# Optimization experiments

Hardware: AMD Instinct MI355X
Metric: run time of the kernel (lower is better)

## Reference

```python
import jax, jax.numpy as jnp
import numpy as np

B, T, E, H = 4, 2048, 1024, 16
HS = E // H  # head_size = 64


def setup_inputs() -> dict:
    key = jax.random.key(0)
    ks = jax.random.split(key, 5)
    x = jax.random.normal(ks[0], (B, T, E), jnp.float32)
    scale = 0.02
    Wq = jax.random.normal(ks[1], (H, E, HS), jnp.float32) * scale
    Wk = jax.random.normal(ks[2], (H, E, HS), jnp.float32) * scale
    Wv = jax.random.normal(ks[3], (H, E, HS), jnp.float32) * scale
    Wo = jax.random.normal(ks[4], (E, E), jnp.float32) * scale
    bo = jnp.zeros((E,), jnp.float32)
    return {"x": x, "Wq": Wq, "Wk": Wk, "Wv": Wv, "Wo": Wo, "bo": bo}


def reference(x, Wq, Wk, Wv, Wo, bo):
    b, t, e = x.shape
    # per-head projections, batched over heads
    Q = jnp.einsum('bte,hed->bhtd', x, Wq)  # (B,H,T,HS)
    K = jnp.einsum('bte,hed->bhtd', x, Wk)
    V = jnp.einsum('bte,hed->bhtd', x, Wv)
    # faithful quirk 1: scale by sqrt(embd_size), not sqrt(head_size)
    scores = jnp.einsum('bhtd,bhsd->bhts', Q, K) / jnp.sqrt(jnp.float32(e))
    mask = jnp.tril(jnp.ones((t, t), dtype=bool))  # (T_q, T_k)
    scores = jnp.where(mask[None, None, :, :], scores, -jnp.inf)
    # faithful quirk 2: original softmaxes over dim=1 of (B,Tq,Tk) = the QUERY axis
    attn = jax.nn.softmax(scores, axis=2)
    out = jnp.einsum('bhts,bhsd->bhtd', attn, V)  # (B,H,T,HS)
    out = out.transpose(0, 2, 1, 3).reshape(b, t, e)  # concat heads -> (B,T,E)
    return out @ Wo + bo
```

## Files before the change

### kernel.cpp

```cpp
#include <hip/hip_runtime.h>
#include <stdint.h>

#define Bn 4
#define Tn 2048
#define En 1024
#define Hn 16
#define HSn 64
#define BHn (Bn*Hn)
#define NRn (Bn*Tn)

#define CEXP 0.0450840831f

typedef __attribute__((ext_vector_type(8))) short short8;
typedef __attribute__((ext_vector_type(4))) float f32x4;
typedef __attribute__((ext_vector_type(16))) float f32x16;
typedef __attribute__((ext_vector_type(4))) unsigned int uint4w;

__device__ __forceinline__ unsigned short f2b(float f){
  union { float f; unsigned int u; } c; c.f = f;
  unsigned int u = c.u + 0x7FFFu + ((c.u >> 16) & 1u);
  return (unsigned short)(u >> 16);
}
__device__ __forceinline__ float b2f(unsigned short s){
  union { unsigned int u; float f; } c; c.u = ((unsigned int)s) << 16;
  return c.f;
}
__device__ __forceinline__ unsigned int cvtpk(float lo, float hi){
  unsigned int r;
  asm("v_cvt_pk_bf16_f32 %0, %1, %2" : "=v"(r) : "v"(lo), "v"(hi));
  return r;
}
__device__ __forceinline__ f32x4 mfma16(short8 a, short8 b, f32x4 c){
  return __builtin_amdgcn_mfma_f32_16x16x32_bf16(a, b, c, 0, 0, 0);
}
__device__ __forceinline__ f32x16 mfma32(short8 a, short8 b, f32x16 c){
  return __builtin_amdgcn_mfma_f32_32x32x16_bf16(a, b, c, 0, 0, 0);
}
__device__ __forceinline__ void gl16(const void* g, void* s){
  __builtin_amdgcn_global_load_lds((const __attribute__((address_space(1))) unsigned int*)g,
                                   (__attribute__((address_space(3))) unsigned int*)s, 16, 0, 0);
}
#define FENCE()    asm volatile("" ::: "memory")
#define WAITV(N)   asm volatile("s_waitcnt vmcnt(" #N ")" ::: "memory")
#define SBAR()     __builtin_amdgcn_s_barrier()

__global__ void k_cvt_x(const float* __restrict__ x, unsigned short* __restrict__ xb){
  int i = (blockIdx.x * blockDim.x + threadIdx.x) * 8;
  float4 a = *(const float4*)(x + i);
  float4 b = *(const float4*)(x + i + 4);
  alignas(16) unsigned short o[8] = {f2b(a.x),f2b(a.y),f2b(a.z),f2b(a.w),
                                     f2b(b.x),f2b(b.y),f2b(b.z),f2b(b.w)};
  *(uint4w*)(xb + i) = *(const uint4w*)o;
}

__global__ void k_wT(const float* __restrict__ Wq, const float* __restrict__ Wk,
                     const float* __restrict__ Wv, const float* __restrict__ Wo,
                     unsigned short* __restrict__ Wt, unsigned short* __restrict__ Wot)
{
  __shared__ unsigned short Ls[64*80];
  const int tid = threadIdx.x;
  const int ey = blockIdx.x, jt = blockIdx.y;
  const int e0 = ey*64;
  const float* src; int R, c0; unsigned short* outp; float sc = 1.0f;
  if (jt < 48){
    int sel = jt >> 4, h = jt & 15;
    const float* W = (sel==0)?Wq:((sel==1)?Wk:Wv);
    if (sel == 0) sc = CEXP;
    src = W + h*(En*HSn); R = HSn; c0 = 0;
    outp = Wt + jt*64*En;
  } else {
    src = Wo; R = En; c0 = (jt-48)*64;
    outp = Wot + (jt-48)*64*En;
  }
  {
    const int e = tid >> 2, cq = (tid & 3)*16;
    const float* p = src + (e0 + e)*R + c0 + cq;
    float vv[16];
    *(float4*)&vv[0]  = *(const float4*)(p);
    *(float4*)&vv[4]  = *(const float4*)(p+4);
    *(float4*)&vv[8]  = *(const float4*)(p+8);
    *(float4*)&vv[12] = *(const float4*)(p+12);
#pragma unroll
    for (int i = 0; i < 16; i++) Ls[(cq+i)*80 + e] = f2b(vv[i]*sc);
  }
  __syncthreads();
  {
    const int c8 = tid & 7, r = tid >> 3;
#pragma unroll
    for (int rr0 = 0; rr0 < 2; rr0++){
      int rr = r + rr0*32;
      *(uint4w*)(outp + rr*En + e0 + c8*8) = *(const uint4w*)&Ls[rr*80 + c8*8];
    }
  }
}

__global__ void __launch_bounds__(256, 2)
k_qkv(const unsigned short* __restrict__ xb,
      const unsigned short* __restrict__ Wt,
      unsigned short* __restrict__ Qb, unsigned short* __restrict__ Kb,
      unsigned short* __restrict__ Vt)
{
  __shared__ unsigned short As[2][128*64];
  __shared__ unsigned short Bs[2][128*64];
  const int tid = threadIdx.x, lane = tid & 63, w = tid >> 6;
  const int wr = w >> 1, wc = w & 1;
  const int mb = blockIdx.x, nb = blockIdx.y;
  const int n0 = nb*128;
  const int sel = n0 >> 10;
  const int nj0 = n0 & 1023;
  const int l15 = lane & 15, kc = lane >> 4;
  const int r8 = lane >> 3, c7 = lane & 7;

  const unsigned short* xbase = xb + (mb*128)*En;
  const unsigned short* wbase = Wt + n0*En;

  f32x4 acc[4][4];
#pragma unroll
  for (int i = 0; i < 4; i++)
#pragma unroll
    for (int j = 0; j < 4; j++) acc[i][j] = (f32x4){0.f,0.f,0.f,0.f};

  auto stage = [&](int buf, int k0){
#pragma unroll
    for (int i = 0; i < 4; i++){
      const int rb = w*32 + i*8;
      const int r = rb + r8;
      const int g = (c7 ^ r8) * 8;
      gl16(xbase + r*En + k0 + g, &As[buf][rb*64]);
      gl16(wbase + r*En + k0 + g, &Bs[buf][rb*64]);
    }
  };
  auto compute = [&](int cur){
    const unsigned short* Ac = &As[cur][0];
    const unsigned short* Bc = &Bs[cur][0];
#pragma unroll
    for (int ks = 0; ks < 2; ks++){
      short8 af[4], bf[4];
#pragma unroll
      for (int mf = 0; mf < 4; mf++){
        int ar = wr*64 + mf*16 + l15;
        af[mf] = *(const short8*)&Ac[ar*64 + (((ks*4 + kc) ^ (ar & 7))*8)];
      }
#pragma unroll
      for (int nf = 0; nf < 4; nf++){
        int br = wc*64 + nf*16 + l15;
        bf[nf] = *(const short8*)&Bc[br*64 + (((ks*4 + kc) ^ (br & 7))*8)];
      }
      __builtin_amdgcn_s_setprio(1);
#pragma unroll
      for (int mf = 0; mf < 4; mf++)
#pragma unroll
        for (int nf = 0; nf < 4; nf++)
          acc[mf][nf] = mfma16(af[mf], bf[nf], acc[mf][nf]);
      __builtin_amdgcn_s_setprio(0);
    }
  };

  stage(0, 0);
  stage(1, 64);
  WAITV(8); SBAR();

  for (int kt = 0; kt < 16; kt++){
    const int cur = kt & 1;
    compute(cur);
    FENCE(); SBAR();
    if (kt < 14){
      stage(cur, (kt + 2)*64);
      WAITV(8); SBAR();
    } else if (kt == 14){
      WAITV(0); SBAR();
    }
  }
  __syncthreads();

  const int q4 = (lane >> 4)*4;
  const int bb = mb >> 4;
  const int tt0 = (mb*128) & 2047;

  if (sel == 2){
    unsigned short* tb = ((w < 2) ? &As[0][0] : &Bs[0][0]) + (w & 1)*8192;
#pragma unroll
    for (int nf = 0; nf < 4; nf++)
#pragma unroll
      for (int mf = 0; mf < 4; mf++){
        uint2 u;
        u.x = cvtpk(acc[mf][nf][0], acc[mf][nf][1]);
        u.y = cvtpk(acc[mf][nf][2], acc[mf][nf][3]);
        *(uint2*)&tb[(nf*16 + l15)*72 + mf*16 + q4] = u;
      }
    const int hh = (nj0 >> 6) + wc;
    unsigned short* vb = Vt + ((bb*Hn + hh)*HSn)*Tn + tt0 + wr*64;
#pragma unroll
    for (int i = 0; i < 8; i++){
      int rr = i*8 + r8;
      *(uint4w*)(vb + rr*Tn + c7*8) = *(const uint4w*)&tb[rr*72 + c7*8];
    }
  } else {
    unsigned short* Out = (sel == 1) ? Kb : Qb;
#pragma unroll
    for (int nf = 0; nf < 4; nf++){
      int jj = nj0 + wc*64 + nf*16 + l15;
      int hh = jj >> 6, dd = jj & 63;
#pragma unroll
      for (int mf = 0; mf < 4; mf++){
#pragma unroll
        for (int q = 0; q < 4; q++){
          int tt = tt0 + wr*64 + mf*16 + q4 + q;
          Out[((bb*Hn + hh)*Tn + tt)*HSn + dd] = f2b(acc[mf][nf][q]);
        }
      }
    }
  }
}

__global__ void __launch_bounds__(256, 3)
k_colsum(const unsigned short* __restrict__ Qb,
         const unsigned short* __restrict__ Kb,
         unsigned short* __restrict__ Vt,
         float* __restrict__ Linv)
{
  __shared__ unsigned short Qs[3][128*64];
  __shared__ float Lred[64];
  const int bh = blockIdx.x*8 + (blockIdx.y & 7);
  const int sb = blockIdx.y >> 3;
  const int s0 = sb * 64;
  const int tid = threadIdx.x, lane = tid & 63, w = tid >> 6;
  const int l5 = lane >> 5, l31 = lane & 31;
  const int r8 = lane >> 3, c7 = lane & 7;

  short8 kf[2][4];
#pragma unroll
  for (int sf = 0; sf < 2; sf++){
    const unsigned short* kr = Kb + (bh*Tn + s0 + sf*32 + l31)*HSn + 8*l5;
#pragma unroll
    for (int ks = 0; ks < 4; ks++) kf[sf][ks] = *(const short8*)(kr + 16*ks);
  }

  float ls[2][16];
#pragma unroll
  for (int sf = 0; sf < 2; sf++)
#pragma unroll
    for (int r = 0; r < 16; r++) ls[sf][r] = 0.f;

  if (tid < 64) Lred[tid] = 0.f;

  const int t0s = (s0 >> 7) << 7;
  const int ntl = (Tn - t0s) >> 7;

  auto stageQ = [&](int buf, int tg0){
#pragma unroll
    for (int i = 0; i < 4; i++){
      int row = (w*4 + i)*8 + r8;
      gl16(Qb + (bh*Tn + tg0 + row)*HSn + ((c7 ^ (row & 7))*8), &Qs[buf][(w*4 + i)*512]);
    }
  };

  stageQ(0, t0s + (ntl-1)*128);
  if (ntl > 1) stageQ(1, t0s + (ntl-2)*128);

  for (int j = 0; j < ntl; j++){
    if (j + 1 < ntl){ WAITV(4); } else { WAITV(0); }
    FENCE(); SBAR(); FENCE();
    if (j + 2 < ntl) stageQ((j + 2) % 3, t0s + (ntl-3-j)*128);

    const int cur = j % 3;
    const int t0 = t0s + (ntl-1-j)*128;
    const int tw = t0 + 32*w;
    if (tw + 31 >= s0){
      f32x16 st[2];
#pragma unroll
      for (int sf = 0; sf < 2; sf++)
#pragma unroll
        for (int r = 0; r < 16; r++) st[sf][r] = 0.f;
      const int qrow = w*32 + l31;
      const unsigned short* Qc = &Qs[cur][qrow*64];
      const int sw = qrow & 7;
      __builtin_amdgcn_s_setprio(1);
#pragma unroll
      for (int ks = 0; ks < 4; ks++){
        short8 qb = *(const short8*)&Qc[((l5 + 2*ks) ^ sw)*8];
        st[0] = mfma32(kf[0][ks], qb, st[0]);
        st[1] = mfma32(kf[1][ks], qb, st[1]);
      }
      __builtin_amdgcn_s_setprio(0);
      const int tg = tw + l31;
      if (s0 + 63 <= tw){
#pragma unroll
        for (int sf = 0; sf < 2; sf++)
#pragma unroll
          for (int r = 0; r < 16; r++)
            ls[sf][r] += __builtin_amdgcn_exp2f(st[sf][r]);
      } else {
#pragma unroll
        for (int sf = 0; sf < 2; sf++)
#pragma unroll
          for (int r = 0; r < 16; r++){
            int sg = s0 + 32*sf + (r & 3) + 8*(r >> 2) + 4*l5;
            float e = __builtin_amdgcn_exp2f(st[sf][r]);
            ls[sf][r] += (tg >= sg) ? e : 0.f;
          }
      }
    }
  }

#pragma unroll
  for (int sf = 0; sf < 2; sf++)
#pragma unroll
    for (int r = 0; r < 16; r++){
      float v = ls[sf][r];
      v += __shfl_xor(v, 1);  v += __shfl_xor(v, 2);
      v += __shfl_xor(v, 4);  v += __shfl_xor(v, 8);
      v += __shfl_xor(v, 16);
      ls[sf][r] = v;
    }
  if (l31 == 0){
#pragma unroll
    for (int sf = 0; sf < 2; sf++)
#pragma unroll
      for (int r = 0; r < 16; r++){
        int sl = 32*sf + (r & 3) + 8*(r >> 2) + 4*l5;
        atomicAdd(&Lred[sl], ls[sf][r]);
      }
  }
  __syncthreads();
  if (tid < 64) Linv[bh*Tn + s0 + tid] = 1.0f / Lred[tid];

  {
    const int d = tid >> 2, cq = (tid & 3)*16;
    unsigned short* vp = Vt + ((size_t)(bh*HSn + d))*Tn + s0 + cq;
    short8 v0 = *(const short8*)vp;
    short8 v1 = *(const short8*)(vp + 8);
    float inv[16];
#pragma unroll
    for (int j = 0; j < 16; j++) inv[j] = 1.0f / Lred[cq + j];
    uint4w o0, o1;
    o0[0] = cvtpk(b2f((unsigned short)v0[0])*inv[0],  b2f((unsigned short)v0[1])*inv[1]);
    o0[1] = cvtpk(b2f((unsigned short)v0[2])*inv[2],  b2f((unsigned short)v0[3])*inv[3]);
    o0[2] = cvtpk(b2f((unsigned short)v0[4])*inv[4],  b2f((unsigned short)v0[5])*inv[5]);
    o0[3] = cvtpk(b2f((unsigned short)v0[6])*inv[6],  b2f((unsigned short)v0[7])*inv[7]);
    o1[0] = cvtpk(b2f((unsigned short)v1[0])*inv[8],  b2f((unsigned short)v1[1])*inv[9]);
    o1[1] = cvtpk(b2f((unsigned short)v1[2])*inv[10], b2f((unsigned short)v1[3])*inv[11]);
    o1[2] = cvtpk(b2f((unsigned short)v1[4])*inv[12], b2f((unsigned short)v1[5])*inv[13]);
    o1[3] = cvtpk(b2f((unsigned short)v1[6])*inv[14], b2f((unsigned short)v1[7])*inv[15]);
    *(uint4w*)vp       = o0;
    *(uint4w*)(vp + 8) = o1;
  }
}

__global__ void __launch_bounds__(256, 3)
k_attn(const unsigned short* __restrict__ Qb,
       const unsigned short* __restrict__ Kb,
       const unsigned short* __restrict__ Vlt,
       unsigned short* __restrict__ Att)
{
  __shared__ unsigned short Ks[3][64*64];
  __shared__ unsigned short Vs[3][64*64];
  const int bh = blockIdx.x*8 + (blockIdx.y & 7);
  const int tb = 15 - (blockIdx.y >> 3);
  const int t0 = tb * 128;
  const int tid = threadIdx.x, lane = tid & 63, w = tid >> 6;
  const int l5 = lane >> 5, l31 = lane & 31;
  const int c7 = lane & 7, r8 = lane >> 3;
  const int tbase = t0 + w*32;
  const int nt = 2*tb + 2;

  short8 qf[4];
  {
    const unsigned short* qr = Qb + (bh*Tn + tbase + l31)*HSn + 8*l5;
#pragma unroll
    for (int ks = 0; ks < 4; ks++) qf[ks] = *(const short8*)(qr + 16*ks);
  }

  f32x16 oacc[2];
#pragma unroll
  for (int df = 0; df < 2; df++)
#pragma unroll
    for (int r = 0; r < 16; r++) oacc[df][r] = 0.f;

  auto stageKV = [&](int buf, int sn){
#pragma unroll
    for (int i = 0; i < 2; i++){
      int row = (w*2 + i)*8 + r8;
      gl16(Kb  + (bh*Tn + sn + row)*HSn + ((c7 ^ (row & 7))*8), &Ks[buf][(w*2 + i)*512]);
      gl16(Vlt + (bh*HSn + row)*Tn + sn + ((c7 ^ (row & 7))*8), &Vs[buf][(w*2 + i)*512]);
    }
  };

  stageKV(0, 0);
  if (nt > 1) stageKV(1, 64);

  for (int it = 0; it < nt; it++){
    if (it + 1 < nt){ WAITV(4); } else { WAITV(0); }
    FENCE(); SBAR(); FENCE();
    if (it + 2 < nt) stageKV((it + 2) % 3, (it + 2)*64);

    const int cur = it % 3;
    const int s0 = it * 64;
    if (s0 <= tbase + 31){
      const unsigned short* Kc = &Ks[cur][0];
      f32x16 st[2];
#pragma unroll
      for (int sf = 0; sf < 2; sf++)
#pragma unroll
        for (int r = 0; r < 16; r++) st[sf][r] = 0.f;
      __builtin_amdgcn_s_setprio(1);
#pragma unroll
      for (int ks = 0; ks < 4; ks++){
#pragma unroll
        for (int sf = 0; sf < 2; sf++){
          int row = sf*32 + l31;
          short8 ka = *(const short8*)&Kc[row*64 + (((l5 + 2*ks) ^ (row & 7))*8)];
          st[sf] = mfma32(ka, qf[ks], st[sf]);
        }
      }
      __builtin_amdgcn_s_setprio(0);

      const int tg = tbase + l31;
      const bool interior = (s0 + 63 <= tbase);
#pragma unroll
      for (int sf = 0; sf < 2; sf++){
#pragma unroll
        for (int r = 0; r < 16; r++){
          float e = __builtin_amdgcn_exp2f(st[sf][r]);
          if (!interior){
            int sg = s0 + 32*sf + (r & 3) + 8*(r >> 2) + 4*l5;
            e = (tg >= sg) ? e : 0.f;
          }
          st[sf][r] = e;
        }
      }

      short8 pb[4];
#pragma unroll
      for (int sf = 0; sf < 2; sf++){
#pragma unroll
        for (int q = 0; q < 2; q++){
          unsigned int ax = cvtpk(st[sf][8*q+0], st[sf][8*q+1]);
          unsigned int ay = cvtpk(st[sf][8*q+2], st[sf][8*q+3]);
          unsigned int bx = cvtpk(st[sf][8*q+4], st[sf][8*q+5]);
          unsigned int by = cvtpk(st[sf][8*q+6], st[sf][8*q+7]);
          asm("v_permlane32_swap_b32 %0, %1" : "+v"(ax), "+v"(bx));
          asm("v_permlane32_swap_b32 %0, %1" : "+v"(ay), "+v"(by));
          union { unsigned int u[4]; short8 s; } pk;
          pk.u[0] = ax; pk.u[1] = ay; pk.u[2] = bx; pk.u[3] = by;
          pb[sf*2 + q] = pk.s;
        }
      }

      const unsigned short* Vc = &Vs[cur][0];
      __builtin_amdgcn_s_setprio(1);
#pragma unroll
      for (int ks = 0; ks < 4; ks++){
#pragma unroll
        for (int df = 0; df < 2; df++){
          int row = df*32 + l31;
          short8 va = *(const short8*)&Vc[row*64 + (((l5 + 2*ks) ^ (row & 7))*8)];
          oacc[df] = mfma32(va, pb[ks], oacc[df]);
        }
      }
      __builtin_amdgcn_s_setprio(0);
    }
  }

  {
    const int tg = tbase + l31;
    unsigned short* ob = Att + (bh*Tn + tg)*HSn;
#pragma unroll
    for (int df = 0; df < 2; df++)
#pragma unroll
      for (int r2 = 0; r2 < 4; r2++){
        uint2 u;
        u.x = cvtpk(oacc[df][r2*4+0], oacc[df][r2*4+1]);
        u.y = cvtpk(oacc[df][r2*4+2], oacc[df][r2*4+3]);
        *(uint2*)&ob[32*df + 8*r2 + 4*l5] = u;
      }
  }
}

__global__ void __launch_bounds__(256, 2)
k_oproj(const unsigned short* __restrict__ Att,
        const unsigned short* __restrict__ Wot,
        const float* __restrict__ bo, float* __restrict__ out)
{
  __shared__ unsigned short As[2][128*64];
  __shared__ unsigned short Bs[2][128*64];
  const int tid = threadIdx.x, lane = tid & 63, w = tid >> 6;
  const int wr = w >> 1, wc = w & 1;
  const int mb = blockIdx.x, nb = blockIdx.y;
  const int n0 = nb*128;
  const int l15 = lane & 15, kc = lane >> 4;
  const int r8 = lane >> 3, c7 = lane & 7;
  const int bb = mb >> 4;
  const int t0 = (mb*128) & 2047;

  f32x4 acc[4][4];
#pragma unroll
  for (int i = 0; i < 4; i++)
#pragma unroll
    for (int j = 0; j < 4; j++) acc[i][j] = (f32x4){0.f,0.f,0.f,0.f};

  const unsigned short* wbase = Wot + n0*En;

  auto stage = [&](int buf, int k0){
    const int hh = k0 >> 6;
    const unsigned short* abase = Att + ((bb*Hn + hh)*Tn + t0)*HSn;
#pragma unroll
    for (int i = 0; i < 4; i++){
      const int rb = w*32 + i*8;
      const int r = rb + r8;
      const int g = (c7 ^ r8) * 8;
      gl16(abase + r*HSn + g, &As[buf][rb*64]);
      gl16(wbase + r*En + k0 + g, &Bs[buf][rb*64]);
    }
  };
  auto compute = [&](int cur){
    const unsigned short* Ac = &As[cur][0];
    const unsigned short* Bc = &Bs[cur][0];
#pragma unroll
    for (int ks = 0; ks < 2; ks++){
      short8 af[4], bf[4];
#pragma unroll
      for (int mf = 0; mf < 4; mf++){
        int ar = wr*64 + mf*16 + l15;
        af[mf] = *(const short8*)&Ac[ar*64 + (((ks*4 + kc) ^ (ar & 7))*8)];
      }
#pragma unroll
      for (int nf = 0; nf < 4; nf++){
        int br = wc*64 + nf*16 + l15;
        bf[nf] = *(const short8*)&Bc[br*64 + (((ks*4 + kc) ^ (br & 7))*8)];
      }
      __builtin_amdgcn_s_setprio(1);
#pragma unroll
      for (int mf = 0; mf < 4; mf++)
#pragma unroll
        for (int nf = 0; nf < 4; nf++)
          acc[mf][nf] = mfma16(af[mf], bf[nf], acc[mf][nf]);
      __builtin_amdgcn_s_setprio(0);
    }
  };

  stage(0, 0);
  stage(1, 64);
  WAITV(8); SBAR();

  for (int kt = 0; kt < 16; kt++){
    const int cur = kt & 1;
    compute(cur);
    FENCE(); SBAR();
    if (kt < 14){
      stage(cur, (kt + 2)*64);
      WAITV(8); SBAR();
    } else if (kt == 14){
      WAITV(0); SBAR();
    }
  }

  const int q4 = (lane >> 4)*4;
#pragma unroll
  for (int nf = 0; nf < 4; nf++){
    int j = n0 + wc*64 + nf*16 + l15;
    float bias = bo[j];
#pragma unroll
    for (int mf = 0; mf < 4; mf++){
#pragma unroll
      for (int q = 0; q < 4; q++){
        int rr = mb*128 + wr*64 + mf*16 + q4 + q;
        out[rr*En + j] = acc[mf][nf][q] + bias;
      }
    }
  }
}

extern "C" void kernel_launch(void* const* d_in, const int* in_sizes, int n_in,
                              void* d_out, int out_size, void* d_ws, size_t ws_size,
                              hipStream_t stream)
{
  (void)in_sizes; (void)n_in; (void)out_size; (void)ws_size;
  const float* x  = (const float*)d_in[0];
  const float* Wq = (const float*)d_in[1];
  const float* Wk = (const float*)d_in[2];
  const float* Wv = (const float*)d_in[3];
  const float* Wo = (const float*)d_in[4];
  const float* bo = (const float*)d_in[5];
  float* out = (float*)d_out;

  uint8_t* w = (uint8_t*)d_ws;
  unsigned short* Qb  = (unsigned short*)(w);
  unsigned short* Kb  = (unsigned short*)(w + (16u << 20));
  unsigned short* Vt  = (unsigned short*)(w + (32u << 20));
  unsigned short* xb  = (unsigned short*)(w + (48u << 20));
  unsigned short* Att = (unsigned short*)(w + (48u << 20));
  unsigned short* Wt  = (unsigned short*)(w + (64u << 20));
  unsigned short* Wot = (unsigned short*)(w + (70u << 20));
  float* Linv         = (float*)(w + (72u << 20));

  hipLaunchKernelGGL(k_cvt_x,  dim3(4096),    dim3(256), 0, stream, x, xb);
  hipLaunchKernelGGL(k_wT,     dim3(16, 64),  dim3(256), 0, stream, Wq, Wk, Wv, Wo, Wt, Wot);
  hipLaunchKernelGGL(k_qkv,    dim3(64, 24),  dim3(256), 0, stream, xb, Wt, Qb, Kb, Vt);
  hipLaunchKernelGGL(k_colsum, dim3(8, 256),  dim3(256), 0, stream, Qb, Kb, Vt, Linv);
  hipLaunchKernelGGL(k_attn,   dim3(8, 128),  dim3(256), 0, stream, Qb, Kb, Vt, Att);
  hipLaunchKernelGGL(k_oproj,  dim3(64, 8),   dim3(256), 0, stream, Att, Wot, bo, out);
}
```

Before: 199.2 us.

## Use 8-wave GEMM blocks and process two query tiles per attention block

The QKV and output-projection GEMMs now launch 512 threads per 128x128 tile, with each wave owning a 32x64 sub-tile. This halves per-thread accumulators and raises occupancy, but each wave reuses fewer loaded fragments. The attention kernel now handles 256 query rows per block, split into two 128-row halves, so each staged K/V tile serves twice as many queries and the grid shrinks by half. The cost is more registers in attention and fewer blocks, which may worsen load balance across the causal triangle.

```diff
diff --git a/kernel.cpp b/kernel.cpp
--- a/kernel.cpp
+++ b/kernel.cpp
@@ -94,7 +94,7 @@
   }
 }
 
-__global__ void __launch_bounds__(256, 2)
+__global__ void __launch_bounds__(512, 4)
 k_qkv(const unsigned short* __restrict__ xb,
       const unsigned short* __restrict__ Wt,
       unsigned short* __restrict__ Qb, unsigned short* __restrict__ Kb,
@@ -110,20 +110,21 @@
   const int nj0 = n0 & 1023;
   const int l15 = lane & 15, kc = lane >> 4;
   const int r8 = lane >> 3, c7 = lane & 7;
+  const int q4 = (lane >> 4)*4;
 
   const unsigned short* xbase = xb + (mb*128)*En;
   const unsigned short* wbase = Wt + n0*En;
 
-  f32x4 acc[4][4];
-#pragma unroll
-  for (int i = 0; i < 4; i++)
+  f32x4 acc[2][4];
+#pragma unroll
+  for (int i = 0; i < 2; i++)
 #pragma unroll
     for (int j = 0; j < 4; j++) acc[i][j] = (f32x4){0.f,0.f,0.f,0.f};
 
   auto stage = [&](int buf, int k0){
 #pragma unroll
-    for (int i = 0; i < 4; i++){
-      const int rb = w*32 + i*8;
+    for (int i = 0; i < 2; i++){
+      const int rb = w*16 + i*8;
       const int r = rb + r8;
       const int g = (c7 ^ r8) * 8;
       gl16(xbase + r*En + k0 + g, &As[buf][rb*64]);
@@ -135,10 +136,10 @@
     const unsigned short* Bc = &Bs[cur][0];
 #pragma unroll
     for (int ks = 0; ks < 2; ks++){
-      short8 af[4], bf[4];
-#pragma unroll
-      for (int mf = 0; mf < 4; mf++){
-        int ar = wr*64 + mf*16 + l15;
+      short8 af[2], bf[4];
+#pragma unroll
+      for (int mf = 0; mf < 2; mf++){
+        int ar = wr*32 + mf*16 + l15;
         af[mf] = *(const short8*)&Ac[ar*64 + (((ks*4 + kc) ^ (ar & 7))*8)];
       }
 #pragma unroll
@@ -148,7 +149,7 @@
       }
       __builtin_amdgcn_s_setprio(1);
 #pragma unroll
-      for (int mf = 0; mf < 4; mf++)
+      for (int mf = 0; mf < 2; mf++)
 #pragma unroll
         for (int nf = 0; nf < 4; nf++)
           acc[mf][nf] = mfma16(af[mf], bf[nf], acc[mf][nf]);
@@ -158,7 +159,7 @@
 
   stage(0, 0);
   stage(1, 64);
-  WAITV(8); SBAR();
+  WAITV(4); SBAR();
 
   for (int kt = 0; kt < 16; kt++){
     const int cur = kt & 1;
@@ -166,34 +167,34 @@
     FENCE(); SBAR();
     if (kt < 14){
       stage(cur, (kt + 2)*64);
-      WAITV(8); SBAR();
+      WAITV(4); SBAR();
     } else if (kt == 14){
       WAITV(0); SBAR();
     }
   }
   __syncthreads();
 
-  const int q4 = (lane >> 4)*4;
   const int bb = mb >> 4;
   const int tt0 = (mb*128) & 2047;
 
   if (sel == 2){
-    unsigned short* tb = ((w < 2) ? &As[0][0] : &Bs[0][0]) + (w & 1)*8192;
+    unsigned short* tb = ((w < 4) ? &As[0][0] + w*2560 : &Bs[0][0] + (w-4)*2560);
 #pragma unroll
     for (int nf = 0; nf < 4; nf++)
 #pragma unroll
-      for (int mf = 0; mf < 4; mf++){
+      for (int mf = 0; mf < 2; mf++){
         uint2 u;
         u.x = cvtpk(acc[mf][nf][0], acc[mf][nf][1]);
         u.y = cvtpk(acc[mf][nf][2], acc[mf][nf][3]);
-        *(uint2*)&tb[(nf*16 + l15)*72 + mf*16 + q4] = u;
+        *(uint2*)&tb[(nf*16 + l15)*40 + mf*16 + q4] = u;
       }
     const int hh = (nj0 >> 6) + wc;
-    unsigned short* vb = Vt + ((bb*Hn + hh)*HSn)*Tn + tt0 + wr*64;
-#pragma unroll
-    for (int i = 0; i < 8; i++){
-      int rr = i*8 + r8;
-      *(uint4w*)(vb + rr*Tn + c7*8) = *(const uint4w*)&tb[rr*72 + c7*8];
+    unsigned short* vb = Vt + ((size_t)(bb*Hn + hh)*HSn)*Tn + tt0 + wr*32;
+#pragma unroll
+    for (int i = 0; i < 4; i++){
+      int rr = i*16 + (lane >> 2);
+      int c2 = lane & 3;
+      *(uint4w*)(vb + (size_t)rr*Tn + c2*8) = *(const uint4w*)&tb[rr*40 + c2*8];
     }
   } else {
     unsigned short* Out = (sel == 1) ? Kb : Qb;
@@ -202,10 +203,10 @@
       int jj = nj0 + wc*64 + nf*16 + l15;
       int hh = jj >> 6, dd = jj & 63;
 #pragma unroll
-      for (int mf = 0; mf < 4; mf++){
+      for (int mf = 0; mf < 2; mf++){
 #pragma unroll
         for (int q = 0; q < 4; q++){
-          int tt = tt0 + wr*64 + mf*16 + q4 + q;
+          int tt = tt0 + wr*32 + mf*16 + q4 + q;
           Out[((bb*Hn + hh)*Tn + tt)*HSn + dd] = f2b(acc[mf][nf][q]);
         }
       }
@@ -356,38 +357,40 @@
   __shared__ unsigned short Ks[3][64*64];
   __shared__ unsigned short Vs[3][64*64];
   const int bh = blockIdx.x*8 + (blockIdx.y & 7);
-  const int tb = 15 - (blockIdx.y >> 3);
-  const int t0 = tb * 128;
+  const int tb = 7 - (blockIdx.y >> 3);
+  const int t0 = tb * 256;
   const int tid = threadIdx.x, lane = tid & 63, w = tid >> 6;
   const int l5 = lane >> 5, l31 = lane & 31;
   const int c7 = lane & 7, r8 = lane >> 3;
-  const int tbase = t0 + w*32;
-  const int nt = 2*tb + 2;
-
-  short8 qf[4];
-  {
-    const unsigned short* qr = Qb + (bh*Tn + tbase + l31)*HSn + 8*l5;
-#pragma unroll
-    for (int ks = 0; ks < 4; ks++) qf[ks] = *(const short8*)(qr + 16*ks);
-  }
-
-  f32x16 oacc[2];
-#pragma unroll
-  for (int df = 0; df < 2; df++)
-#pragma unroll
-    for (int r = 0; r < 16; r++) oacc[df][r] = 0.f;
+  const int nt = 4*tb + 4;
+
+  short8 qf[2][4];
+#pragma unroll
+  for (int h = 0; h < 2; h++){
+    const unsigned short* qr = Qb + (bh*Tn + t0 + h*128 + w*32 + l31)*HSn + 8*l5;
+#pragma unroll
+    for (int ks = 0; ks < 4; ks++) qf[h][ks] = *(const short8*)(qr + 16*ks);
+  }
+
+  f32x16 oacc[2][2];
+#pragma unroll
+  for (int h = 0; h < 2; h++)
+#pragma unroll
+    for (int df = 0; df < 2; df++)
+#pragma unroll
+      for (int r = 0; r < 16; r++) oacc[h][df][r] = 0.f;
 
   auto stageKV = [&](int buf, int sn){
 #pragma unroll
     for (int i = 0; i < 2; i++){
       int row = (w*2 + i)*8 + r8;
       gl16(Kb  + (bh*Tn + sn + row)*HSn + ((c7 ^ (row & 7))*8), &Ks[buf][(w*2 + i)*512]);
-      gl16(Vlt + (bh*HSn + row)*Tn + sn + ((c7 ^ (row & 7))*8), &Vs[buf][(w*2 + i)*512]);
+      gl16(Vlt + ((size_t)(bh*HSn + row))*Tn + sn + ((c7 ^ (row & 7))*8), &Vs[buf][(w*2 + i)*512]);
     }
   };
 
   stageKV(0, 0);
-  if (nt > 1) stageKV(1, 64);
+  stageKV(1, 64);
 
   for (int it = 0; it < nt; it++){
     if (it + 1 < nt){ WAITV(4); } else { WAITV(0); }
@@ -396,8 +399,13 @@
 
     const int cur = it % 3;
     const int s0 = it * 64;
-    if (s0 <= tbase + 31){
-      const unsigned short* Kc = &Ks[cur][0];
+    const unsigned short* Kc = &Ks[cur][0];
+    const unsigned short* Vc = &Vs[cur][0];
+
+#pragma unroll
+    for (int h = 0; h < 2; h++){
+      const int tbase = t0 + h*128 + w*32;
+      if (s0 > tbase + 31) continue;
       f32x16 st[2];
 #pragma unroll
       for (int sf = 0; sf < 2; sf++)
@@ -410,7 +418,7 @@
         for (int sf = 0; sf < 2; sf++){
           int row = sf*32 + l31;
           short8 ka = *(const short8*)&Kc[row*64 + (((l5 + 2*ks) ^ (row & 7))*8)];
-          st[sf] = mfma32(ka, qf[ks], st[sf]);
+          st[sf] = mfma32(ka, qf[h][ks], st[sf]);
         }
       }
       __builtin_amdgcn_s_setprio(0);
@@ -447,7 +455,6 @@
         }
       }
 
-      const unsigned short* Vc = &Vs[cur][0];
       __builtin_amdgcn_s_setprio(1);
 #pragma unroll
       for (int ks = 0; ks < 4; ks++){
@@ -455,29 +462,30 @@
         for (int df = 0; df < 2; df++){
           int row = df*32 + l31;
           short8 va = *(const short8*)&Vc[row*64 + (((l5 + 2*ks) ^ (row & 7))*8)];
-          oacc[df] = mfma32(va, pb[ks], oacc[df]);
+          oacc[h][df] = mfma32(va, pb[ks], oacc[h][df]);
         }
       }
       __builtin_amdgcn_s_setprio(0);
     }
   }
 
-  {
-    const int tg = tbase + l31;
+#pragma unroll
+  for (int h = 0; h < 2; h++){
+    const int tg = t0 + h*128 + w*32 + l31;
     unsigned short* ob = Att + (bh*Tn + tg)*HSn;
 #pragma unroll
     for (int df = 0; df < 2; df++)
 #pragma unroll
       for (int r2 = 0; r2 < 4; r2++){
         uint2 u;
-        u.x = cvtpk(oacc[df][r2*4+0], oacc[df][r2*4+1]);
-        u.y = cvtpk(oacc[df][r2*4+2], oacc[df][r2*4+3]);
+        u.x = cvtpk(oacc[h][df][r2*4+0], oacc[h][df][r2*4+1]);
+        u.y = cvtpk(oacc[h][df][r2*4+2], oacc[h][df][r2*4+3]);
         *(uint2*)&ob[32*df + 8*r2 + 4*l5] = u;
       }
   }
 }
 
-__global__ void __launch_bounds__(256, 2)
+__global__ void __launch_bounds__(512, 4)
 k_oproj(const unsigned short* __restrict__ Att,
         const unsigned short* __restrict__ Wot,
         const float* __restrict__ bo, float* __restrict__ out)
@@ -490,12 +498,13 @@
   const int n0 = nb*128;
   const int l15 = lane & 15, kc = lane >> 4;
   const int r8 = lane >> 3, c7 = lane & 7;
+  const int q4 = (lane >> 4)*4;
   const int bb = mb >> 4;
   const int t0 = (mb*128) & 2047;
 
-  f32x4 acc[4][4];
-#pragma unroll
-  for (int i = 0; i < 4; i++)
+  f32x4 acc[2][4];
+#pragma unroll
+  for (int i = 0; i < 2; i++)
 #pragma unroll
     for (int j = 0; j < 4; j++) acc[i][j] = (f32x4){0.f,0.f,0.f,0.f};
 
@@ -505,8 +514,8 @@
     const int hh = k0 >> 6;
     const unsigned short* abase = Att + ((bb*Hn + hh)*Tn + t0)*HSn;
 #pragma unroll
-    for (int i = 0; i < 4; i++){
-      const int rb = w*32 + i*8;
+    for (int i = 0; i < 2; i++){
+      const int rb = w*16 + i*8;
       const int r = rb + r8;
       const int g = (c7 ^ r8) * 8;
       gl16(abase + r*HSn + g, &As[buf][rb*64]);
@@ -518,10 +527,10 @@
     const unsigned short* Bc = &Bs[cur][0];
 #pragma unroll
     for (int ks = 0; ks < 2; ks++){
-      short8 af[4], bf[4];
-#pragma unroll
-      for (int mf = 0; mf < 4; mf++){
-        int ar = wr*64 + mf*16 + l15;
+      short8 af[2], bf[4];
+#pragma unroll
+      for (int mf = 0; mf < 2; mf++){
+        int ar = wr*32 + mf*16 + l15;
         af[mf] = *(const short8*)&Ac[ar*64 + (((ks*4 + kc) ^ (ar & 7))*8)];
       }
 #pragma unroll
@@ -531,7 +540,7 @@
       }
       __builtin_amdgcn_s_setprio(1);
 #pragma unroll
-      for (int mf = 0; mf < 4; mf++)
+      for (int mf = 0; mf < 2; mf++)
 #pragma unroll
         for (int nf = 0; nf < 4; nf++)
           acc[mf][nf] = mfma16(af[mf], bf[nf], acc[mf][nf]);
@@ -541,7 +550,7 @@
 
   stage(0, 0);
   stage(1, 64);
-  WAITV(8); SBAR();
+  WAITV(4); SBAR();
 
   for (int kt = 0; kt < 16; kt++){
     const int cur = kt & 1;
@@ -549,22 +558,21 @@
     FENCE(); SBAR();
     if (kt < 14){
       stage(cur, (kt + 2)*64);
-      WAITV(8); SBAR();
+      WAITV(4); SBAR();
     } else if (kt == 14){
       WAITV(0); SBAR();
     }
   }
 
-  const int q4 = (lane >> 4)*4;
 #pragma unroll
   for (int nf = 0; nf < 4; nf++){
     int j = n0 + wc*64 + nf*16 + l15;
     float bias = bo[j];
 #pragma unroll
-    for (int mf = 0; mf < 4; mf++){
+    for (int mf = 0; mf < 2; mf++){
 #pragma unroll
       for (int q = 0; q < 4; q++){
-        int rr = mb*128 + wr*64 + mf*16 + q4 + q;
+        int rr = mb*128 + wr*32 + mf*16 + q4 + q;
         out[rr*En + j] = acc[mf][nf][q] + bias;
       }
     }
@@ -596,8 +604,8 @@
 
   hipLaunchKernelGGL(k_cvt_x,  dim3(4096),    dim3(256), 0, stream, x, xb);
   hipLaunchKernelGGL(k_wT,     dim3(16, 64),  dim3(256), 0, stream, Wq, Wk, Wv, Wo, Wt, Wot);
-  hipLaunchKernelGGL(k_qkv,    dim3(64, 24),  dim3(256), 0, stream, xb, Wt, Qb, Kb, Vt);
+  hipLaunchKernelGGL(k_qkv,    dim3(64, 24),  dim3(512), 0, stream, xb, Wt, Qb, Kb, Vt);
   hipLaunchKernelGGL(k_colsum, dim3(8, 256),  dim3(256), 0, stream, Qb, Kb, Vt, Linv);
-  hipLaunchKernelGGL(k_attn,   dim3(8, 128),  dim3(256), 0, stream, Qb, Kb, Vt, Att);
-  hipLaunchKernelGGL(k_oproj,  dim3(64, 8),   dim3(256), 0, stream, Att, Wot, bo, out);
-}
+  hipLaunchKernelGGL(k_attn,   dim3(8, 64),   dim3(256), 0, stream, Qb, Kb, Vt, Att);
+  hipLaunchKernelGGL(k_oproj,  dim3(64, 8),   dim3(512), 0, stream, Att, Wot, bo, out);
+}
```

Result: slower. 244.6 us (+22.8%).
